# Optimization experiments

Hardware: AMD Instinct MI355X
Metric: run time of the kernel (lower is better)

The kernel has to match this reference:

```python
import jax, jax.numpy as jnp
import numpy as np

D = 512      # d_model
H = 8        # n_heads
DK = D // H  # head dim
F = 2048     # d_ff
K = 31       # depthwise kernel size
B = 8
T = 1024
LN_EPS = 1e-5
BN_EPS = 1e-5


def setup_inputs() -> dict:
    key = jax.random.key(0)
    ks = jax.random.split(key, 24)
    def nrm(k, shape, scale=0.02):
        return jax.random.normal(k, shape, jnp.float32) * scale
    d = {
        'x': jax.random.normal(ks[0], (B, T, D), jnp.float32),
        # FF1
        'ff1_ln_g': jnp.ones((D,), jnp.float32), 'ff1_ln_b': jnp.zeros((D,), jnp.float32),
        'ff1_w1': nrm(ks[1], (D, F)), 'ff1_b1': jnp.zeros((F,), jnp.float32),
        'ff1_w2': nrm(ks[2], (F, D)), 'ff1_b2': jnp.zeros((D,), jnp.float32),
        # Attention
        'attn_ln_g': jnp.ones((D,), jnp.float32), 'attn_ln_b': jnp.zeros((D,), jnp.float32),
        'wq': nrm(ks[3], (D, D)), 'bq': jnp.zeros((D,), jnp.float32),
        'wk': nrm(ks[4], (D, D)), 'bk': jnp.zeros((D,), jnp.float32),
        'wv': nrm(ks[5], (D, D)), 'bv': jnp.zeros((D,), jnp.float32),
        'wo': nrm(ks[6], (D, D)), 'bo': jnp.zeros((D,), jnp.float32),
        # Conv module
        'conv_ln_g': jnp.ones((D,), jnp.float32), 'conv_ln_b': jnp.zeros((D,), jnp.float32),
        'pw1_w': nrm(ks[7], (D, 2 * D)), 'pw1_b': jnp.zeros((2 * D,), jnp.float32),
        'dw_w': nrm(ks[8], (D, K)), 'dw_b': jnp.zeros((D,), jnp.float32),
        'bn_g': jnp.ones((D,), jnp.float32), 'bn_b': jnp.zeros((D,), jnp.float32),
        'bn_mean': jnp.zeros((D,), jnp.float32), 'bn_var': jnp.ones((D,), jnp.float32),
        'pw2_w': nrm(ks[9], (D, D)), 'pw2_b': jnp.zeros((D,), jnp.float32),
        # FF2
        'ff2_ln_g': jnp.ones((D,), jnp.float32), 'ff2_ln_b': jnp.zeros((D,), jnp.float32),
        'ff2_w1': nrm(ks[10], (D, F)), 'ff2_b1': jnp.zeros((F,), jnp.float32),
        'ff2_w2': nrm(ks[11], (F, D)), 'ff2_b2': jnp.zeros((D,), jnp.float32),
        # Final norm
        'final_ln_g': jnp.ones((D,), jnp.float32), 'final_ln_b': jnp.zeros((D,), jnp.float32),
    }
    return d


def _ln(x, g, b):
    m = jnp.mean(x, axis=-1, keepdims=True)
    v = jnp.mean(jnp.square(x - m), axis=-1, keepdims=True)
    return (x - m) * jax.lax.rsqrt(v + LN_EPS) * g + b


def _swish(x):
    return x * jax.nn.sigmoid(x)


def _ffn(x, g, b, w1, b1, w2, b2):
    h = _swish(_ln(x, g, b) @ w1 + b1)
    return h @ w2 + b2


def _block(x, ff1_ln_g, ff1_ln_b, ff1_w1, ff1_b1, ff1_w2, ff1_b2,
           attn_ln_g, attn_ln_b, wq, bq, wk, bk, wv, bv, wo, bo,
           conv_ln_g, conv_ln_b, pw1_w, pw1_b, dw_w, dw_b,
           bn_g, bn_b, bn_mean, bn_var, pw2_w, pw2_b,
           ff2_ln_g, ff2_ln_b, ff2_w1, ff2_b1, ff2_w2, ff2_b2,
           final_ln_g, final_ln_b):
    # FF1 half-residual
    x = x + 0.5 * _ffn(x, ff1_ln_g, ff1_ln_b, ff1_w1, ff1_b1, ff1_w2, ff1_b2)

    # Multi-head self-attention (mask=None)
    y = _ln(x, attn_ln_g, attn_ln_b)
    q = (y @ wq + bq).reshape(B, T, H, DK)
    k = (y @ wk + bk).reshape(B, T, H, DK)
    v = (y @ wv + bv).reshape(B, T, H, DK)
    scores = jnp.einsum('bqhd,bkhd->bhqk', q, k) / np.sqrt(DK).astype(np.float32)
    attn = jax.nn.softmax(scores, axis=-1)
    o = jnp.einsum('bhqk,bkhd->bqhd', attn, v).reshape(B, T, D)
    x = x + (o @ wo + bo)

    # Convolution module: LN -> pw1 -> GLU -> depthwise -> BN(eval) -> Swish -> pw2
    y = _ln(x, conv_ln_g, conv_ln_b)
    y = y @ pw1_w + pw1_b                      # [B,T,2D]
    a, g = y[..., :D], y[..., D:]
    y = a * jax.nn.sigmoid(g)                  # GLU over channels
    yt = jnp.transpose(y, (0, 2, 1))           # [B,D,T]
    yt = jax.lax.conv_general_dilated(
        yt, dw_w[:, None, :],                  # kernel [D,1,K]
        window_strides=(1,), padding=[(K // 2, K // 2)],
        feature_group_count=D,
        dimension_numbers=('NCH', 'OIH', 'NCH')) + dw_b[None, :, None]
    yt = (yt - bn_mean[None, :, None]) * jax.lax.rsqrt(bn_var + BN_EPS)[None, :, None]
    yt = yt * bn_g[None, :, None] + bn_b[None, :, None]
    yt = _swish(yt)
    y = jnp.transpose(yt, (0, 2, 1)) @ pw2_w + pw2_b
    x = x + y

    # FF2 half-residual
    x = x + 0.5 * _ffn(x, ff2_ln_g, ff2_ln_b, ff2_w1, ff2_b1, ff2_w2, ff2_b2)
    return _ln(x, final_ln_g, final_ln_b)


def reference(x, ff1_ln_g, ff1_ln_b, ff1_w1, ff1_b1, ff1_w2, ff1_b2,
              attn_ln_g, attn_ln_b, wq, bq, wk, bk, wv, bv, wo, bo,
              conv_ln_g, conv_ln_b, pw1_w, pw1_b, dw_w, dw_b,
              bn_g, bn_b, bn_mean, bn_var, pw2_w, pw2_b,
              ff2_ln_g, ff2_ln_b, ff2_w1, ff2_b1, ff2_w2, ff2_b2,
              final_ln_g, final_ln_b):
    return _block(x, ff1_ln_g, ff1_ln_b, ff1_w1, ff1_b1, ff1_w2, ff1_b2,
                  attn_ln_g, attn_ln_b, wq, bq, wk, bk, wv, bv, wo, bo,
                  conv_ln_g, conv_ln_b, pw1_w, pw1_b, dw_w, dw_b,
                  bn_g, bn_b, bn_mean, bn_var, pw2_w, pw2_b,
                  ff2_ln_g, ff2_ln_b, ff2_w1, ff2_b1, ff2_w2, ff2_b2,
                  final_ln_g, final_ln_b)
```

## Files before the change

kernel.cpp:

```cpp
#include <hip/hip_runtime.h>
#include <cstdint>
#include <cstddef>


typedef __attribute__((ext_vector_type(8))) short bf16x8;
typedef __attribute__((ext_vector_type(4))) float f32x4;
typedef unsigned short u16;

#define DEV static __device__ __forceinline__

DEV float bf2f(u16 u) { union { unsigned int i; float f; } x; x.i = ((unsigned int)u) << 16; return x.f; }
DEV u16 f2bf(float f) {
    union { float f; unsigned int i; } x; x.f = f;
    unsigned int r = x.i + 0x7fffu + ((x.i >> 16) & 1u);
    return (u16)(r >> 16);
}
DEV float sigm(float x) { return 1.f / (1.f + __expf(-x)); }
DEV unsigned cvt_pk_bf16(float lo, float hi) {
    unsigned r;
    asm("v_cvt_pk_bf16_f32 %0, %1, %2" : "=v"(r) : "v"(lo), "v"(hi));
    return r;
}

#define GLL16(GP, LP) __builtin_amdgcn_global_load_lds( \
    (__attribute__((address_space(1))) void*)(GP),      \
    (__attribute__((address_space(3))) void*)(LP), 16, 0, 0)

DEV const bf16x8* lds_rd(const u16* buf, int r, int s) {
    return (const bf16x8*)((const char*)buf + r * 64 + ((s ^ ((r >> 1) & 3)) << 4));
}

template <int F32IN>
DEV void ld8(const void* p, size_t off, float* v) {
    if constexpr (F32IN) {
        *(float4*)(v) = *(const float4*)((const float*)p + off);
        *(float4*)(v + 4) = *(const float4*)((const float*)p + off + 4);
    } else {
        const bf16x8 u = *(const bf16x8*)((const u16*)p + off);
#pragma unroll
        for (int j = 0; j < 8; j++) v[j] = bf2f((u16)u[j]);
    }
}

struct CastJob { const float* in; u16* out; int K, M, tile0, rmp; };
struct CastJobs {
    CastJob j[11];
    const float* lnx; const float* lng; const float* lnb; u16* lnout;
};

__global__ __launch_bounds__(256) void k_castall(CastJobs J) {
    __shared__ float t[32][33];
    const int bid = blockIdx.x;
    const int tid = threadIdx.y * 32 + threadIdx.x;
    if (bid >= J.j[10].tile0) {
        const int row = (bid - J.j[10].tile0) * 4 + (tid >> 6);
        const int l = tid & 63;
        const size_t base = (size_t)row * 512 + l * 8;
        float v[8];
        ld8<1>(J.lnx, base, v);
        float s = 0.f;
#pragma unroll
        for (int j = 0; j < 8; j++) s += v[j];
#pragma unroll
        for (int m = 1; m < 64; m <<= 1) s += __shfl_xor(s, m);
        const float mean = s * (1.f / 512.f);
        float ss = 0.f;
#pragma unroll
        for (int j = 0; j < 8; j++) { v[j] -= mean; ss += v[j] * v[j]; }
#pragma unroll
        for (int m = 1; m < 64; m <<= 1) ss += __shfl_xor(ss, m);
        const float rs = rsqrtf(ss * (1.f / 512.f) + 1e-5f);
        float gv[8], bv[8];
        *(float4*)(gv) = *(const float4*)(J.lng + l * 8);
        *(float4*)(gv + 4) = *(const float4*)(J.lng + l * 8 + 4);
        *(float4*)(bv) = *(const float4*)(J.lnb + l * 8);
        *(float4*)(bv + 4) = *(const float4*)(J.lnb + l * 8 + 4);
        union { u16 u[8]; bf16x8 v8; } o;
#pragma unroll
        for (int j = 0; j < 8; j++) o.u[j] = f2bf(v[j] * rs * gv[j] + bv[j]);
        *(bf16x8*)(J.lnout + base) = o.v8;
        return;
    }
    int ji = 0;
    while (bid >= J.j[ji + 1].tile0) ++ji;
    const CastJob job = J.j[ji];
    const int tIdx = bid - job.tile0;
    const int tilesX = job.M >> 5;
    const int m0 = (tIdx % tilesX) * 32, k0 = (tIdx / tilesX) * 32;
    const int lx = threadIdx.x, ly = threadIdx.y;
#pragma unroll
    for (int i = 0; i < 4; i++) {
        const int kk = ly + i * 8;
        t[kk][lx] = job.in[(size_t)(k0 + kk) * job.M + m0 + lx];
    }
    __syncthreads();
#pragma unroll
    for (int i = 0; i < 4; i++) {
        const int mm = ly + i * 8;
        const int m = m0 + mm;
        const int mr = job.rmp ? ((((m & 511) >> 4) << 5) + ((m >> 9) << 4) + (m & 15)) : m;
        job.out[(size_t)mr * job.K + k0 + lx] = f2bf(t[lx][mm]);
    }
}

template <int MODE, int RESF32>
__global__ __launch_bounds__(256) void k_mergeln(const u16* __restrict__ p,
                                                 const void* __restrict__ resid,
                                                 const float* __restrict__ bias,
                                                 const float scale,
                                                 const float* __restrict__ g,
                                                 const float* __restrict__ bt,
                                                 u16* __restrict__ xout,
                                                 void* __restrict__ lnout) {
    const int row = blockIdx.x * 4 + (threadIdx.x >> 6);
    const int l = threadIdx.x & 63;
    const size_t base = (size_t)row * 512 + l * 8;
    float p0[8], p1[8], rv[8], bv[8], v[8];
    ld8<0>(p, base, p0);
    ld8<0>(p + 4194304, base, p1);
    ld8<RESF32>(resid, base, rv);
    *(float4*)(bv) = *(const float4*)(bias + l * 8);
    *(float4*)(bv + 4) = *(const float4*)(bias + l * 8 + 4);
#pragma unroll
    for (int j = 0; j < 8; j++) v[j] = rv[j] + scale * (p0[j] + p1[j] + bv[j]);
    if constexpr (MODE == 0) {
        union { u16 u[8]; bf16x8 v8; } xo;
#pragma unroll
        for (int j = 0; j < 8; j++) xo.u[j] = f2bf(v[j]);
        *(bf16x8*)(xout + base) = xo.v8;
    }
    float s = 0.f;
#pragma unroll
    for (int j = 0; j < 8; j++) s += v[j];
#pragma unroll
    for (int m = 1; m < 64; m <<= 1) s += __shfl_xor(s, m);
    const float mean = s * (1.f / 512.f);
    float ss = 0.f;
#pragma unroll
    for (int j = 0; j < 8; j++) { v[j] -= mean; ss += v[j] * v[j]; }
#pragma unroll
    for (int m = 1; m < 64; m <<= 1) ss += __shfl_xor(ss, m);
    const float rs = rsqrtf(ss * (1.f / 512.f) + 1e-5f);
    float gv[8], btv[8];
    *(float4*)(gv) = *(const float4*)(g + l * 8);
    *(float4*)(gv + 4) = *(const float4*)(g + l * 8 + 4);
    *(float4*)(btv) = *(const float4*)(bt + l * 8);
    *(float4*)(btv + 4) = *(const float4*)(bt + l * 8 + 4);
    if constexpr (MODE == 1) {
        float o[8];
#pragma unroll
        for (int j = 0; j < 8; j++) o[j] = v[j] * rs * gv[j] + btv[j];
        float* op = (float*)lnout + base;
        *(float4*)(op) = *(float4*)(o);
        *(float4*)(op + 4) = *(float4*)(o + 4);
    } else {
        union { u16 u[8]; bf16x8 v8; } o;
#pragma unroll
        for (int j = 0; j < 8; j++) o.u[j] = f2bf(v[j] * rs * gv[j] + btv[j]);
        *(bf16x8*)((u16*)lnout + base) = o.v8;
    }
}

template <int EP, int BN, int NBUF = 3, int WAVES = 4, int MINW = 1>
__global__ __launch_bounds__(WAVES * 64, MINW) void k_gemm(const u16* __restrict__ A,
                                              const u16* __restrict__ Bt,
                                              const int Kstr, const int kcount,
                                              const int M,
                                              const float* __restrict__ bias,
                                              const void* __restrict__ resid,
                                              const float scale,
                                              void* __restrict__ outp,
                                              const float* __restrict__ bias2,
                                              const float* __restrict__ bias3) {
    constexpr int CPW = BN / (WAVES / 2);
    constexpr int NI = CPW / 16;
    constexpr int ACH = 8 / WAVES ? 8 / WAVES : 1;
    constexpr int BCH = (BN / 16) / WAVES;
    constexpr int LPW = ACH + BCH;
    __shared__ __align__(16) u16 sA[NBUF][128 * 32];
    __shared__ __align__(16) u16 sB[NBUF][BN * 32];
    const int tid = threadIdx.x, w = tid >> 6, l = tid & 63;
    const int wr = (WAVES == 4 ? (w >> 1) : (w >> 2)) * 64;
    const int wc = (WAVES == 4 ? (w & 1) : (w & 3)) * CPW;
    const int bm = blockIdx.x * 128, bn = blockIdx.y * BN;
    const int kbase = (EP == 4) ? blockIdx.z * kcount : 0;
    const int l15 = l & 15, ls = l >> 4;
    const int lrow = l >> 2, lslot = l & 3;
    const int NT = kcount >> 5;
    f32x4 acc[4][NI] = {};

#define STAGE(BUF, T)                                                          \
    {                                                                          \
        _Pragma("unroll") for (int i = 0; i < ACH; i++) {                      \
            const int c = w * ACH + i;                                         \
            const int r = c * 16 + lrow;                                       \
            const int sl = lslot ^ ((r >> 1) & 3);                             \
            GLL16(A + (size_t)(bm + r) * Kstr + kbase + (T) * 32 + sl * 8,     \
                  (char*)sA[BUF] + c * 1024);                                  \
        }                                                                      \
        _Pragma("unroll") for (int i = 0; i < BCH; i++) {                      \
            const int c = w * BCH + i;                                         \
            const int r = c * 16 + lrow;                                       \
            const int sl = lslot ^ ((r >> 1) & 3);                             \
            GLL16(Bt + (size_t)(bn + r) * Kstr + kbase + (T) * 32 + sl * 8,    \
                  (char*)sB[BUF] + c * 1024);                                  \
        }                                                                      \
    }

#define WAITC(N)                                                               \
    {                                                                          \
        if constexpr (N == 2) asm volatile("s_waitcnt vmcnt(2)" ::: "memory"); \
        else if constexpr (N == 3) asm volatile("s_waitcnt vmcnt(3)" ::: "memory"); \
        else asm volatile("s_waitcnt vmcnt(4)" ::: "memory");                  \
    }

#define COMPUTE(BUF)                                                           \
    {                                                                          \
        bf16x8 af[4], bfr[NI];                                                 \
        _Pragma("unroll") for (int i = 0; i < 4; i++)                          \
            af[i] = *lds_rd(&sA[BUF][0], wr + i * 16 + l15, ls);               \
        _Pragma("unroll") for (int i = 0; i < NI; i++)                         \
            bfr[i] = *lds_rd(&sB[BUF][0], wc + i * 16 + l15, ls);              \
        __builtin_amdgcn_s_setprio(1);                                         \
        _Pragma("unroll") for (int mi = 0; mi < 4; mi++)                       \
            _Pragma("unroll") for (int ni = 0; ni < NI; ni++)                  \
                acc[mi][ni] = __builtin_amdgcn_mfma_f32_16x16x32_bf16(         \
                    af[mi], bfr[ni], acc[mi][ni], 0, 0, 0);                    \
        __builtin_amdgcn_s_setprio(0);                                         \
    }

    if constexpr (NBUF == 2) {
        STAGE(0, 0);
        int cur = 0;
        for (int t = 0; t < NT; ++t) {
            if (t + 1 < NT) {
                STAGE(cur ^ 1, t + 1);
                WAITC(LPW);
            } else {
                asm volatile("s_waitcnt vmcnt(0)" ::: "memory");
            }
            __builtin_amdgcn_s_barrier();
            __builtin_amdgcn_sched_barrier(0);
            COMPUTE(cur);
            __builtin_amdgcn_s_barrier();
            cur ^= 1;
        }
    } else {
        STAGE(0, 0);
        if (NT > 1) STAGE(1, 1);
        int cur = 0;
        for (int t = 0; t < NT; ++t) {
            if (t + 1 < NT) {
                WAITC(LPW);
            } else {
                asm volatile("s_waitcnt vmcnt(0)" ::: "memory");
            }
            __builtin_amdgcn_s_barrier();
            __builtin_amdgcn_sched_barrier(0);
            const int nxt = (cur >= 1) ? cur - 1 : cur + 2;
            if (t + 2 < NT) STAGE(nxt, t + 2);
            COMPUTE(cur);
            cur = (cur + 1 == 3) ? 0 : cur + 1;
        }
    }
#undef STAGE
#undef WAITC
#undef COMPUTE

    if constexpr (EP == 5) {
        const int creal = ((bn + wc) >> 1) + l15;
        const float ba = bias[creal], bg = bias[creal + 512];
        const int r0e = bm + wr + ls * 4;
#pragma unroll
        for (int mi = 0; mi < 4; mi++)
#pragma unroll
            for (int j = 0; j < 4; j++) {
                const int row = r0e + mi * 16 + j;
                const float a = acc[mi][0][j] + ba;
                const float g = acc[mi][1][j] + bg;
                ((u16*)outp)[(size_t)row * 512 + creal] = f2bf(a * sigm(g));
            }
        return;
    }

    if constexpr (EP == 3) {
        if (bn >= 1024) {
            __syncthreads();
            u16* EPB = (wc & 64) ? (u16*)sB : (u16*)sA;
#pragma unroll
            for (int ni = 0; ni < NI; ni++) {
                const int cc = (wc & 63) + ni * 16 + l15;
                const int cglob = (bn - 1024) + wc + ni * 16 + l15;
                const float b3 = bias3[cglob];
#pragma unroll
                for (int mp = 0; mp < 2; mp++) {
                    unsigned pk[4];
#pragma unroll
                    for (int j = 0; j < 4; j++)
                        pk[j] = cvt_pk_bf16(acc[mp * 2][ni][j] + b3, acc[mp * 2 + 1][ni][j] + b3);
                    const int panel = (wr >> 5) + mp;
                    const int off = (panel * 64 + ls * 16) ^ ((cc & 7) << 4);
                    *(bf16x8*)((char*)EPB + cc * 256 + off) = *(bf16x8*)pk;
                }
            }
            __syncthreads();
            const int b_ = bm >> 10, tp0 = (bm & 1023) >> 5;
            u16* vout = (u16*)outp + 8388608;
            constexpr int VI = 2048 / (WAVES * 64);
#pragma unroll
            for (int i = 0; i < VI; i++) {
                const int combo = i * ((WAVES * 64) / 256) + (tid >> 8);
                const int head = combo & 1, panel = combo >> 1;
                const int t8 = tid & 255;
                const int dk = t8 >> 2, sub = t8 & 3;
                const u16* SRC = head ? (u16*)sB : (u16*)sA;
                const int off = (panel * 64 + sub * 16) ^ ((dk & 7) << 4);
                const bf16x8 vv = *(const bf16x8*)((const char*)SRC + dk * 256 + off);
                const int hg = ((bn - 1024) >> 6) + head;
                *(bf16x8*)(vout + ((size_t)(b_ * 8 + hg)) * 65536 + (size_t)(tp0 + panel) * 2048 +
                           dk * 32 + sub * 8) = vv;
            }
        } else {
            __syncthreads();
            u16* W = ((w < 4) ? (u16*)sA : (u16*)sB) + (w & 3) * 2560;
            const int c0 = bn + wc;
            const bool isk = c0 >= 512;
            const int cc = isk ? c0 - 512 : c0;
            const int h = cc >> 6, panel = (cc >> 5) & 1;
#pragma unroll
            for (int ni = 0; ni < NI; ni++) {
                const int cglob = c0 + ni * 16 + l15;
                const float bb = isk ? bias2[cglob - 512] : bias[cglob];
#pragma unroll
                for (int mi = 0; mi < 4; mi++)
#pragma unroll
                    for (int j = 0; j < 4; j++) {
                        const int tl = mi * 16 + ls * 4 + j;
                        float v = acc[mi][ni][j] + bb;
                        if (!isk) v *= 0.125f;
                        W[tl * 40 + ni * 16 + l15] = f2bf(v);
                    }
            }
            const int b_ = bm >> 10;
            const int tb = (bm & 1023) + wr;
            u16* dst = (u16*)outp + (isk ? 4194304 : 0) +
                       ((size_t)(b_ * 8 + h)) * 65536 + (size_t)panel * 32768 +
                       (size_t)(tb + l) * 32;
            const u16* src = W + l * 40;
#pragma unroll
            for (int i = 0; i < 4; i++)
                *(bf16x8*)(dst + i * 8) = *(const bf16x8*)(src + i * 8);
        }
        return;
    }

    const int r0 = bm + wr + (l >> 4) * 4;
    const int c0 = bn + wc + l15;
#pragma unroll
    for (int mi = 0; mi < 4; mi++) {
#pragma unroll
        for (int ni = 0; ni < NI; ni++) {
            const int col = c0 + ni * 16;
#pragma unroll
            for (int j = 0; j < 4; j++) {
                const int row = r0 + mi * 16 + j;
                float v = acc[mi][ni][j];
                if constexpr (EP == 0) {
                    v += bias[col];
                    ((u16*)outp)[(size_t)row * M + col] = f2bf(v);
                } else if constexpr (EP == 1) {
                    v += bias[col];
                    v = v * sigm(v);
                    ((u16*)outp)[(size_t)row * M + col] = f2bf(v);
                } else if constexpr (EP == 2) {
                    v += bias[col];
                    const size_t idx = (size_t)row * 512 + col;
                    ((u16*)outp)[idx] = f2bf(bf2f(((const u16*)resid)[idx]) + scale * v);
                } else if constexpr (EP == 4) {
                    ((u16*)outp)[(size_t)blockIdx.z * 4194304 + (size_t)row * 512 + col] = f2bf(v);
                }
            }
        }
    }
}

__global__ __launch_bounds__(512, 6) void k_attn(const u16* __restrict__ qg,
                                              const u16* __restrict__ kg,
                                              const u16* __restrict__ vg,
                                              u16* __restrict__ og) {
    __shared__ __align__(16) u16 sK[2][4096];
    __shared__ __align__(16) u16 sV[2][4096];
    __shared__ __align__(16) char sP[8][32 * 80];
    const int tid = threadIdx.x, w = tid >> 6, l = tid & 63;
    const int bh = blockIdx.x, q0 = blockIdx.y * 128;
    const int b_ = bh >> 3, h = bh & 7;
    const int l15 = l & 15, ls = l >> 4;
    const u16* qh = qg + (size_t)bh * 65536;
    const u16* kh = kg + (size_t)bh * 65536;
    const u16* vh = vg + (size_t)bh * 65536;
    char* myP = &sP[w][0];
    bf16x8 aq[2];
#pragma unroll
    for (int kk = 0; kk < 2; kk++)
        aq[kk] = *(const bf16x8*)(qh + (size_t)kk * 32768 + (q0 + w * 16 + l15) * 32 + ls * 8);
    f32x4 oacc[4] = {};
    float lI[4] = {0.f, 0.f, 0.f, 0.f};

#define ASTAGE(BUF, KT)                                                         \
    {                                                                           \
        const int r = w * 16 + (l >> 2);                                        \
        const int sl = (l & 3) ^ ((r >> 1) & 3);                                \
        GLL16(kh + (size_t)(r >> 6) * 32768 + ((KT) * 64 + (r & 63)) * 32 + sl * 8, \
              (char*)sK[BUF] + w * 1024);                                       \
        GLL16(vh + (size_t)(KT) * 4096 + r * 32 + sl * 8, (char*)sV[BUF] + w * 1024); \
    }

    ASTAGE(0, 0);
    __syncthreads();
    int cur = 0;
    for (int kt = 0; kt < 16; kt++) {
        if (kt + 1 < 16) ASTAGE(cur ^ 1, kt + 1);
        f32x4 s[4] = {};
        __builtin_amdgcn_s_setprio(1);
#pragma unroll
        for (int kk = 0; kk < 2; kk++)
#pragma unroll
            for (int ni = 0; ni < 4; ni++) {
                const bf16x8 kb = *lds_rd(&sK[cur][0], kk * 64 + ni * 16 + l15, ls);
                s[ni] = __builtin_amdgcn_mfma_f32_16x16x32_bf16(aq[kk], kb, s[ni], 0, 0, 0);
            }
        __builtin_amdgcn_s_setprio(0);
#pragma unroll
        for (int ni = 0; ni < 4; ni++)
#pragma unroll
            for (int j = 0; j < 4; j++) {
                const float p = __expf(s[ni][j]);
                s[ni][j] = p;
                lI[j] += p;
            }
#pragma unroll
        for (int kp = 0; kp < 2; kp++)
#pragma unroll
            for (int j = 0; j < 4; j++) {
                const unsigned pk = cvt_pk_bf16(s[kp * 2][j], s[kp * 2 + 1][j]);
                *(unsigned*)(myP + (kp * 16 + ls * 4 + j) * 80 + l15 * 4) = pk;
            }
        __builtin_amdgcn_s_setprio(1);
#pragma unroll
        for (int kp = 0; kp < 2; kp++) {
            const bf16x8 pa = *(const bf16x8*)(myP + (kp * 16 + l15) * 80 + ls * 16);
#pragma unroll
            for (int no = 0; no < 4; no++) {
                const bf16x8 vb = *lds_rd(&sV[cur][0], kp * 64 + no * 16 + l15, ls);
                oacc[no] = __builtin_amdgcn_mfma_f32_16x16x32_bf16(pa, vb, oacc[no], 0, 0, 0);
            }
        }
        __builtin_amdgcn_s_setprio(0);
        __syncthreads();
        cur ^= 1;
    }
#undef ASTAGE
    float rl[4];
#pragma unroll
    for (int j = 0; j < 4; j++) {
        float lt = lI[j];
        lt += __shfl_xor(lt, 1);
        lt += __shfl_xor(lt, 2);
        lt += __shfl_xor(lt, 4);
        lt += __shfl_xor(lt, 8);
        rl[j] = 1.f / lt;
    }
#pragma unroll
    for (int no = 0; no < 4; no++)
#pragma unroll
        for (int j = 0; j < 4; j++) {
            const int t = q0 + w * 16 + ls * 4 + j;
            og[((size_t)b_ * 1024 + t) * 512 + h * 64 + no * 16 + l15] = f2bf(oacc[no][j] * rl[j]);
        }
}

__global__ __launch_bounds__(256) void k_dwconv(const u16* __restrict__ yg,
                                                const float* __restrict__ w,
                                                const float* __restrict__ wb,
                                                const float* __restrict__ bng,
                                                const float* __restrict__ bnb,
                                                const float* __restrict__ bnm,
                                                const float* __restrict__ bnv,
                                                u16* __restrict__ out) {
    __shared__ float tile[158][64];
    __shared__ float wlds[31][64];
    const int b = blockIdx.x, t0 = blockIdx.y * 128, d0 = blockIdx.z * 64;
    const int tid = threadIdx.x;
    for (int s = tid; s < 31 * 64; s += 256) {
        const int k = s >> 6, c = s & 63;
        wlds[k][c] = w[(d0 + c) * 31 + k];
    }
    for (int s = tid; s < 158 * 8; s += 256) {
        const int rr = s >> 3, c8 = s & 7;
        const int t = t0 - 15 + rr;
        float v[8];
        if ((unsigned)t < 1024u) {
            const bf16x8 va = *(const bf16x8*)(yg + ((size_t)b * 1024 + t) * 512 + d0 + c8 * 8);
#pragma unroll
            for (int j = 0; j < 8; j++) v[j] = bf2f((u16)va[j]);
        } else {
#pragma unroll
            for (int j = 0; j < 8; j++) v[j] = 0.f;
        }
        const int cs = ((c8 + (rr >> 1)) & 7) * 8;
        *(float4*)&tile[rr][cs] = *(float4*)v;
        *(float4*)&tile[rr][cs + 4] = *(float4*)(v + 4);
    }
    __syncthreads();
    const int dgrp = tid & 7;
    const int tseg = tid >> 3;
    float acc[4][8] = {};
    float qq[4][8];
#pragma unroll
    for (int j = 0; j < 4; j++) {
        const int row = tseg * 4 + j;
        const int cs = ((dgrp + (row >> 1)) & 7) * 8;
        *(float4*)&qq[j][0] = *(float4*)&tile[row][cs];
        *(float4*)&qq[j][4] = *(float4*)&tile[row][cs + 4];
    }
#pragma unroll
    for (int k = 0; k < 31; k++) {
        float wv[8];
        *(float4*)wv = *(float4*)&wlds[k][dgrp * 8];
        *(float4*)(wv + 4) = *(float4*)&wlds[k][dgrp * 8 + 4];
#pragma unroll
        for (int j = 0; j < 4; j++) {
            const float* xq = qq[(k + j) & 3];
#pragma unroll
            for (int c = 0; c < 8; c++) acc[j][c] += xq[c] * wv[c];
        }
        if (k < 30) {
            const int row = tseg * 4 + k + 4;
            const int cs = ((dgrp + (row >> 1)) & 7) * 8;
            float* xq = qq[k & 3];
            *(float4*)&xq[0] = *(float4*)&tile[row][cs];
            *(float4*)&xq[4] = *(float4*)&tile[row][cs + 4];
        }
    }
    const int d = d0 + dgrp * 8;
    float scl[8], shf[8];
#pragma unroll
    for (int c = 0; c < 8; c++) {
        scl[c] = bng[d + c] * rsqrtf(bnv[d + c] + 1e-5f);
        shf[c] = bnb[d + c] + (wb[d + c] - bnm[d + c]) * scl[c];
    }
#pragma unroll
    for (int j = 0; j < 4; j++) {
        const int t = t0 + tseg * 4 + j;
        union { u16 u[8]; bf16x8 v8; } o;
#pragma unroll
        for (int c = 0; c < 8; c++) {
            float v = acc[j][c] * scl[c] + shf[c];
            o.u[c] = f2bf(v * sigm(v));
        }
        *(bf16x8*)(out + ((size_t)b * 1024 + t) * 512 + d) = o.v8;
    }
}

extern "C" void kernel_launch(void* const* d_in, const int* in_sizes, int n_in,
                              void* d_out, int out_size, void* d_ws, size_t ws_size,
                              hipStream_t stream) {
    (void)in_sizes; (void)n_in; (void)out_size; (void)ws_size;
    const float* x         = (const float*)d_in[0];
    const float* ff1_ln_g  = (const float*)d_in[1];
    const float* ff1_ln_b  = (const float*)d_in[2];
    const float* ff1_w1    = (const float*)d_in[3];
    const float* ff1_b1    = (const float*)d_in[4];
    const float* ff1_w2    = (const float*)d_in[5];
    const float* ff1_b2    = (const float*)d_in[6];
    const float* attn_ln_g = (const float*)d_in[7];
    const float* attn_ln_b = (const float*)d_in[8];
    const float* wq        = (const float*)d_in[9];
    const float* bq        = (const float*)d_in[10];
    const float* wk        = (const float*)d_in[11];
    const float* bk        = (const float*)d_in[12];
    const float* wv        = (const float*)d_in[13];
    const float* bv        = (const float*)d_in[14];
    const float* wo        = (const float*)d_in[15];
    const float* bo        = (const float*)d_in[16];
    const float* conv_ln_g = (const float*)d_in[17];
    const float* conv_ln_b = (const float*)d_in[18];
    const float* pw1_w     = (const float*)d_in[19];
    const float* pw1_b     = (const float*)d_in[20];
    const float* dw_w      = (const float*)d_in[21];
    const float* dw_b      = (const float*)d_in[22];
    const float* bn_g      = (const float*)d_in[23];
    const float* bn_b      = (const float*)d_in[24];
    const float* bn_mean   = (const float*)d_in[25];
    const float* bn_var    = (const float*)d_in[26];
    const float* pw2_w     = (const float*)d_in[27];
    const float* pw2_b     = (const float*)d_in[28];
    const float* ff2_ln_g  = (const float*)d_in[29];
    const float* ff2_ln_b  = (const float*)d_in[30];
    const float* ff2_w1    = (const float*)d_in[31];
    const float* ff2_b1    = (const float*)d_in[32];
    const float* ff2_w2    = (const float*)d_in[33];
    const float* ff2_b2    = (const float*)d_in[34];
    const float* fin_ln_g  = (const float*)d_in[35];
    const float* fin_ln_b  = (const float*)d_in[36];

    char* wsb = (char*)d_ws;
    u16*  W_ff1w1 = (u16*)(wsb + ((size_t)0 << 20));
    u16*  W_ff1w2 = (u16*)(wsb + ((size_t)2 << 20));
    u16*  W_qkv   = (u16*)(wsb + ((size_t)4 << 20));
    u16*  W_wo    = (u16*)(wsb + ((size_t)6 << 20));
    u16*  W_pw1   = (u16*)(wsb + ((size_t)7 << 20));
    u16*  W_pw2   = (u16*)(wsb + ((size_t)8 << 20));
    u16*  W_ff2w1 = (u16*)(wsb + ((size_t)9 << 20));
    u16*  W_ff2w2 = (u16*)(wsb + ((size_t)11 << 20));
    u16*   xcur   = (u16*)(wsb + ((size_t)13 << 20));
    u16*  actA    = (u16*)(wsb + ((size_t)29 << 20));
    u16*  actB    = (u16*)(wsb + ((size_t)37 << 20));
    u16*  PART    = (u16*)(wsb + ((size_t)70 << 20));

    CastJobs J;
    auto setj = [&](int i, const float* in, u16* out, int K, int M, int rmp = 0) {
        J.j[i].in = in; J.j[i].out = out; J.j[i].K = K; J.j[i].M = M; J.j[i].rmp = rmp;
    };
    setj(0, ff1_w1, W_ff1w1, 512, 2048);
    setj(1, ff1_w2, W_ff1w2, 2048, 512);
    setj(2, wq, W_qkv,          512, 512);
    setj(3, wk, W_qkv + 262144, 512, 512);
    setj(4, wv, W_qkv + 524288, 512, 512);
    setj(5, wo, W_wo, 512, 512);
    setj(6, pw1_w, W_pw1, 512, 1024, 1);
    setj(7, pw2_w, W_pw2, 512, 512);
    setj(8, ff2_w1, W_ff2w1, 512, 2048);
    setj(9, ff2_w2, W_ff2w2, 2048, 512);
    int tot = 0;
    for (int i = 0; i < 10; i++) {
        J.j[i].tile0 = tot;
        tot += (J.j[i].M >> 5) * (J.j[i].K >> 5);
    }
    J.j[10].tile0 = tot;
    J.lnx = x; J.lng = ff1_ln_g; J.lnb = ff1_ln_b; J.lnout = actA;
    k_castall<<<tot + 2048, dim3(32, 8), 0, stream>>>(J);

    k_gemm<1, 256, 3, 8, 4><<<dim3(64, 8), 512, 0, stream>>>(actA, W_ff1w1, 512, 512, 2048, ff1_b1, nullptr, 0.f, actB, nullptr, nullptr);
    k_gemm<4, 128, 3, 8, 6><<<dim3(64, 4, 2), 512, 0, stream>>>(actB, W_ff1w2, 2048, 1024, 512, nullptr, nullptr, 0.f, PART, nullptr, nullptr);
    k_mergeln<0, 1><<<2048, 256, 0, stream>>>(PART, x, ff1_b2, 0.5f, attn_ln_g, attn_ln_b, xcur, actA);
    k_gemm<3, 128, 3, 8, 6><<<dim3(64, 12), 512, 0, stream>>>(actA, W_qkv, 512, 512, 1536, bq, nullptr, 0.f, actB, bk, bv);
    k_attn<<<dim3(64, 8), 512, 0, stream>>>(actB, actB + 4194304, actB + 8388608, actA);
    k_gemm<4, 128, 3, 8, 6><<<dim3(64, 4, 2), 512, 0, stream>>>(actA, W_wo, 512, 256, 512, nullptr, nullptr, 0.f, PART, nullptr, nullptr);
    k_mergeln<0, 0><<<2048, 256, 0, stream>>>(PART, xcur, bo, 1.f, conv_ln_g, conv_ln_b, xcur, actA);
    k_gemm<5, 128, 3, 8, 6><<<dim3(64, 8), 512, 0, stream>>>(actA, W_pw1, 512, 512, 512, pw1_b, nullptr, 0.f, actB, nullptr, nullptr);
    k_dwconv<<<dim3(8, 8, 8), 256, 0, stream>>>(actB, dw_w, dw_b, bn_g, bn_b, bn_mean, bn_var, actA);
    k_gemm<4, 128, 3, 8, 6><<<dim3(64, 4, 2), 512, 0, stream>>>(actA, W_pw2, 512, 256, 512, nullptr, nullptr, 0.f, PART, nullptr, nullptr);
    k_mergeln<0, 0><<<2048, 256, 0, stream>>>(PART, xcur, pw2_b, 1.f, ff2_ln_g, ff2_ln_b, xcur, actA);
    k_gemm<1, 256, 3, 8, 4><<<dim3(64, 8), 512, 0, stream>>>(actA, W_ff2w1, 512, 512, 2048, ff2_b1, nullptr, 0.f, actB, nullptr, nullptr);
    k_gemm<4, 128, 3, 8, 6><<<dim3(64, 4, 2), 512, 0, stream>>>(actB, W_ff2w2, 2048, 1024, 512, nullptr, nullptr, 0.f, PART, nullptr, nullptr);
    k_mergeln<1, 0><<<2048, 256, 0, stream>>>(PART, xcur, ff2_b2, 0.5f, fin_ln_g, fin_ln_b, nullptr, d_out);
}
```

Baseline: 255.8 us.

## Triple-buffer attention K/V loads with one barrier; pre-transpose depthwise conv weights

The attention kernel moves from double to triple buffering of K/V tiles in LDS. It prefetches two tiles ahead and replaces the two __syncthreads per iteration with a single vmcnt wait plus s_barrier, so more of the global load latency can overlap with compute. This raises LDS use per block and lowers the occupancy hint from 6 to 4. Separately, the cast kernel gets one extra block that transposes the depthwise conv weights into a [K][D] layout, so the dwconv kernel's weight loads become coalesced.

```diff
diff --git a/kernel.cpp b/kernel.cpp
--- a/kernel.cpp
+++ b/kernel.cpp
@@ -46,12 +46,20 @@
 struct CastJobs {
     CastJob j[11];
     const float* lnx; const float* lng; const float* lnb; u16* lnout;
+    const float* dww; float* dwt;
 };
 
 __global__ __launch_bounds__(256) void k_castall(CastJobs J) {
     __shared__ float t[32][33];
     const int bid = blockIdx.x;
     const int tid = threadIdx.y * 32 + threadIdx.x;
+    if (bid >= J.j[10].tile0 + 2048) {
+        for (int dd = tid; dd < 512; dd += 256) {
+#pragma unroll
+            for (int k = 0; k < 31; k++) J.dwt[k * 512 + dd] = J.dww[dd * 31 + k];
+        }
+        return;
+    }
     if (bid >= J.j[10].tile0) {
         const int row = (bid - J.j[10].tile0) * 4 + (tid >> 6);
         const int l = tid & 63;
@@ -384,12 +392,12 @@
     }
 }
 
-__global__ __launch_bounds__(512, 6) void k_attn(const u16* __restrict__ qg,
+__global__ __launch_bounds__(512, 4) void k_attn(const u16* __restrict__ qg,
                                               const u16* __restrict__ kg,
                                               const u16* __restrict__ vg,
                                               u16* __restrict__ og) {
-    __shared__ __align__(16) u16 sK[2][4096];
-    __shared__ __align__(16) u16 sV[2][4096];
+    __shared__ __align__(16) u16 sK[3][4096];
+    __shared__ __align__(16) u16 sV[3][4096];
     __shared__ __align__(16) char sP[8][32 * 80];
     const int tid = threadIdx.x, w = tid >> 6, l = tid & 63;
     const int bh = blockIdx.x, q0 = blockIdx.y * 128;
@@ -416,10 +424,17 @@
     }
 
     ASTAGE(0, 0);
-    __syncthreads();
+    ASTAGE(1, 1);
     int cur = 0;
     for (int kt = 0; kt < 16; kt++) {
-        if (kt + 1 < 16) ASTAGE(cur ^ 1, kt + 1);
+        if (kt + 1 < 16) asm volatile("s_waitcnt vmcnt(2)" ::: "memory");
+        else             asm volatile("s_waitcnt vmcnt(0)" ::: "memory");
+        __builtin_amdgcn_s_barrier();
+        __builtin_amdgcn_sched_barrier(0);
+        if (kt + 2 < 16) {
+            const int nxt = (cur >= 1) ? cur - 1 : cur + 2;
+            ASTAGE(nxt, kt + 2);
+        }
         f32x4 s[4] = {};
         __builtin_amdgcn_s_setprio(1);
 #pragma unroll
@@ -456,8 +471,7 @@
             }
         }
         __builtin_amdgcn_s_setprio(0);
-        __syncthreads();
-        cur ^= 1;
+        cur = (cur + 1 == 3) ? 0 : cur + 1;
     }
 #undef ASTAGE
     float rl[4];
@@ -493,7 +507,7 @@
     const int tid = threadIdx.x;
     for (int s = tid; s < 31 * 64; s += 256) {
         const int k = s >> 6, c = s & 63;
-        wlds[k][c] = w[(d0 + c) * 31 + k];
+        wlds[k][c] = w[k * 512 + d0 + c];
     }
     for (int s = tid; s < 158 * 8; s += 256) {
         const int rr = s >> 3, c8 = s & 7;
@@ -614,6 +628,7 @@
     u16*  W_ff2w1 = (u16*)(wsb + ((size_t)9 << 20));
     u16*  W_ff2w2 = (u16*)(wsb + ((size_t)11 << 20));
     u16*   xcur   = (u16*)(wsb + ((size_t)13 << 20));
+    float* W_dwt  = (float*)(wsb + ((size_t)21 << 20));
     u16*  actA    = (u16*)(wsb + ((size_t)29 << 20));
     u16*  actB    = (u16*)(wsb + ((size_t)37 << 20));
     u16*  PART    = (u16*)(wsb + ((size_t)70 << 20));
@@ -639,7 +654,8 @@
     }
     J.j[10].tile0 = tot;
     J.lnx = x; J.lng = ff1_ln_g; J.lnb = ff1_ln_b; J.lnout = actA;
-    k_castall<<<tot + 2048, dim3(32, 8), 0, stream>>>(J);
+    J.dww = dw_w; J.dwt = W_dwt;
+    k_castall<<<tot + 2048 + 1, dim3(32, 8), 0, stream>>>(J);
 
     k_gemm<1, 256, 3, 8, 4><<<dim3(64, 8), 512, 0, stream>>>(actA, W_ff1w1, 512, 512, 2048, ff1_b1, nullptr, 0.f, actB, nullptr, nullptr);
     k_gemm<4, 128, 3, 8, 6><<<dim3(64, 4, 2), 512, 0, stream>>>(actB, W_ff1w2, 2048, 1024, 512, nullptr, nullptr, 0.f, PART, nullptr, nullptr);
@@ -649,7 +665,7 @@
     k_gemm<4, 128, 3, 8, 6><<<dim3(64, 4, 2), 512, 0, stream>>>(actA, W_wo, 512, 256, 512, nullptr, nullptr, 0.f, PART, nullptr, nullptr);
     k_mergeln<0, 0><<<2048, 256, 0, stream>>>(PART, xcur, bo, 1.f, conv_ln_g, conv_ln_b, xcur, actA);
     k_gemm<5, 128, 3, 8, 6><<<dim3(64, 8), 512, 0, stream>>>(actA, W_pw1, 512, 512, 512, pw1_b, nullptr, 0.f, actB, nullptr, nullptr);
-    k_dwconv<<<dim3(8, 8, 8), 256, 0, stream>>>(actB, dw_w, dw_b, bn_g, bn_b, bn_mean, bn_var, actA);
+    k_dwconv<<<dim3(8, 8, 8), 256, 0, stream>>>(actB, W_dwt, dw_b, bn_g, bn_b, bn_mean, bn_var, actA);
     k_gemm<4, 128, 3, 8, 6><<<dim3(64, 4, 2), 512, 0, stream>>>(actA, W_pw2, 512, 256, 512, nullptr, nullptr, 0.f, PART, nullptr, nullptr);
     k_mergeln<0, 0><<<2048, 256, 0, stream>>>(PART, xcur, pw2_b, 1.f, ff2_ln_g, ff2_ln_b, xcur, actA);
     k_gemm<1, 256, 3, 8, 4><<<dim3(64, 8), 512, 0, stream>>>(actA, W_ff2w1, 512, 512, 2048, ff2_b1, nullptr, 0.f, actB, nullptr, nullptr);
```

New measurement: 261.4 us. 1.02x slower.
